# Kernel optimization log

Hardware: AMD Instinct MI355X
Metric: run time of the kernel (lower is better)

Reference implementation:

```python
import jax, jax.numpy as jnp
import numpy as np

B, L, D, DI, DS, DC, DTR = 128, 31, 1024, 2048, 16, 5, 64

def setup_inputs() -> dict:
    key = jax.random.key(0)
    ks = jax.random.split(key, 12)
    rn = lambda k, shp, s=0.02: jax.random.normal(k, shp, dtype=jnp.float32) * s
    return {
        "x": jax.random.normal(ks[0], (B, L, D), dtype=jnp.float32),
        "norm1_w": jnp.ones((D,), jnp.float32), "norm1_b": jnp.zeros((D,), jnp.float32),
        "in_proj_W": rn(ks[1], (2 * DI, D)),
        "conv_w": rn(ks[2], (DI, DC), 0.2), "conv_b": jnp.zeros((DI,), jnp.float32),
        "x_proj_W": rn(ks[3], (DTR + 2 * DS, DI)),
        "dt_proj_W": rn(ks[4], (DI, DTR), 0.1),
        "dt_proj_b": jnp.full((DI,), -4.6, dtype=jnp.float32),  # softplus^-1(~0.01)
        "A_log": jnp.tile(jnp.log(jnp.arange(1, DS + 1, dtype=jnp.float32))[None, :], (DI, 1)),
        "D_ssm": jnp.ones((DI,), jnp.float32),
        "out_proj_W": rn(ks[5], (D, DI)),
        "norm2_w": jnp.ones((D,), jnp.float32), "norm2_b": jnp.zeros((D,), jnp.float32),
        "ffn_W1": rn(ks[6], (2 * D, D)), "ffn_b1": jnp.zeros((2 * D,), jnp.float32),
        "ffn_W2": rn(ks[7], (D, 2 * D)), "ffn_b2": jnp.zeros((D,), jnp.float32),
        "cls_W1": rn(ks[8], (D, L * D)), "cls_b1": jnp.zeros((D,), jnp.float32),
        "cls_W2": rn(ks[9], (1, D)), "cls_b2": jnp.zeros((1,), jnp.float32),
    }

def _ln(x, w, b):
    m = x.mean(-1, keepdims=True)
    v = x.var(-1, keepdims=True)
    return (x - m) * jax.lax.rsqrt(v + 1e-5) * w + b

def _mamba(x, in_proj_W, conv_w, conv_b, x_proj_W, dt_proj_W, dt_proj_b, A_log, D_ssm, out_proj_W):
    # in_proj -> (u, z)
    xz = jnp.einsum('bld,ed->ble', x, in_proj_W)            # (B,L,2*DI)
    u, z = jnp.split(xz, 2, axis=-1)
    # causal depthwise conv1d (kernel DC) + SiLU
    xp = jnp.pad(u, ((0, 0), (DC - 1, 0), (0, 0)))
    uc = conv_b + sum(xp[:, k:k + L, :] * conv_w[:, k] for k in range(DC))
    uc = jax.nn.silu(uc)
    # input-dependent dt, B, C
    x_dbl = jnp.einsum('bld,ed->ble', uc, x_proj_W)         # (B,L,DTR+2*DS)
    dt, Bm, Cm = jnp.split(x_dbl, [DTR, DTR + DS], axis=-1)
    dt = jax.nn.softplus(jnp.einsum('blr,dr->bld', dt, dt_proj_W) + dt_proj_b)
    A = -jnp.exp(A_log)                                      # (DI,DS)
    def step(h, ins):
        dt_t, B_t, C_t, u_t = ins                            # (B,DI),(B,DS),(B,DS),(B,DI)
        dA = jnp.exp(dt_t[:, :, None] * A)                   # (B,DI,DS)
        h = h * dA + dt_t[:, :, None] * B_t[:, None, :] * u_t[:, :, None]
        y = jnp.einsum('bds,bs->bd', h, C_t)
        return h, y
    h0 = jnp.zeros((u.shape[0], DI, DS), u.dtype)
    _, ys = jax.lax.scan(step, h0, (dt.transpose(1, 0, 2), Bm.transpose(1, 0, 2),
                                    Cm.transpose(1, 0, 2), uc.transpose(1, 0, 2)))
    y = ys.transpose(1, 0, 2) + uc * D_ssm                   # skip term D*u
    y = y * jax.nn.silu(z)                                   # gate
    return jnp.einsum('bld,ed->ble', y, out_proj_W)

def reference(x, norm1_w, norm1_b, in_proj_W, conv_w, conv_b, x_proj_W, dt_proj_W,
              dt_proj_b, A_log, D_ssm, out_proj_W, norm2_w, norm2_b, ffn_W1, ffn_b1,
              ffn_W2, ffn_b2, cls_W1, cls_b1, cls_W2, cls_b2):
    # single encoder block (n_layers=1), dropout = identity (eval)
    res = x
    h = _ln(x, norm1_w, norm1_b)
    h = _mamba(h, in_proj_W, conv_w, conv_b, x_proj_W, dt_proj_W, dt_proj_b,
               A_log, D_ssm, out_proj_W)
    x = res + h
    res = x
    h = _ln(x, norm2_w, norm2_b)
    h = jax.nn.silu(jnp.einsum('bld,ed->ble', h, ffn_W1) + ffn_b1)
    h = jnp.einsum('ble,de->bld', h, ffn_W2) + ffn_b2
    x = res + h
    # classifier: Flatten -> Linear -> SiLU -> Linear
    flat = x.reshape(x.shape[0], -1)                          # (B, L*D)
    c = jax.nn.silu(flat @ cls_W1.T + cls_b1)
    out = c @ cls_W2.T + cls_b2                               # (B,1)
    return (out, x)
```

## Files before the change

### kernel.cpp

```cpp
#include <hip/hip_runtime.h>
#include <cstddef>
#include <cstdint>

#define B_   128
#define L_   31
#define D_   1024
#define DI_  2048
#define DS_  16
#define DC_  5
#define DTR_ 64
#define ROWS (B_ * L_)
#define KCLS (L_ * D_)

#define W_IN  0
#define W_OUT 4194304
#define W_F1  6291456
#define W_F2  8388608
#define W_XP  10485760
#define W_DT  10747904
#define WTOT  10878976

typedef unsigned short u16;
typedef __attribute__((ext_vector_type(8))) short s16x8;
typedef __attribute__((ext_vector_type(4))) float f32x4;

__device__ __forceinline__ float silu_f(float x) { return x / (1.0f + __expf(-x)); }

__device__ __forceinline__ u16 f2b(float f) {
    union { float f; uint32_t u; } c; c.f = f;
    uint32_t u = c.u + 0x7FFF + ((c.u >> 16) & 1);
    return (u16)(u >> 16);
}
__device__ __forceinline__ float b2f(u16 b) {
    union { uint32_t u; float f; } c; c.u = ((uint32_t)b) << 16;
    return c.f;
}
__device__ __forceinline__ uint32_t pack2(float lo, float hi) {
    return (uint32_t)f2b(lo) | ((uint32_t)f2b(hi) << 16);
}
__device__ __forceinline__ void cvt8(const float* __restrict__ s, u16* __restrict__ d) {
    const float4* p = (const float4*)s;
    float4 a = p[0], b = p[1];
    uint4 r;
    r.x = pack2(a.x, a.y); r.y = pack2(a.z, a.w);
    r.z = pack2(b.x, b.y); r.w = pack2(b.z, b.w);
    *(uint4*)d = r;
}

#define GLD16(g, s) __builtin_amdgcn_global_load_lds( \
    (const __attribute__((address_space(1))) void*)(g), \
    (__attribute__((address_space(3))) void*)(s), 16, 0, 0)

__global__ __launch_bounds__(256) void f2b_all_kernel(
    const float* __restrict__ inW, const float* __restrict__ outW,
    const float* __restrict__ f1W, const float* __restrict__ f2W,
    const float* __restrict__ xpW, const float* __restrict__ dtW,
    u16* __restrict__ wbuf)
{
    int g = blockIdx.x * 256 + threadIdx.x;
    if (g < 524288) { cvt8(inW + (size_t)g * 8, wbuf + W_IN + (size_t)g * 8); return; }
    g -= 524288;
    if (g < 262144) { cvt8(outW + (size_t)g * 8, wbuf + W_OUT + (size_t)g * 8); return; }
    g -= 262144;
    if (g < 262144) { cvt8(f1W + (size_t)g * 8, wbuf + W_F1 + (size_t)g * 8); return; }
    g -= 262144;
    if (g < 262144) { cvt8(f2W + (size_t)g * 8, wbuf + W_F2 + (size_t)g * 8); return; }
    g -= 262144;
    if (g < 32768) {
        const int row = g >> 8, col8 = (g & 255) * 8;
        u16* d = wbuf + W_XP + (size_t)row * 2048 + col8;
        if (row < 96) cvt8(xpW + (size_t)row * 2048 + col8, d);
        else *(uint4*)d = make_uint4(0, 0, 0, 0);
        return;
    }
    g -= 32768;
    if (g < 16384) cvt8(dtW + (size_t)g * 8, wbuf + W_DT + (size_t)g * 8);
}

__global__ __launch_bounds__(256) void ln_kernel(const float* __restrict__ x,
                                                 const float* __restrict__ w,
                                                 const float* __restrict__ b,
                                                 u16* __restrict__ y)
{
    const int row = blockIdx.x;
    const float* xr = x + (size_t)row * D_;
    float v[4];
    float sum = 0.f, sq = 0.f;
#pragma unroll
    for (int i = 0; i < 4; i++) {
        v[i] = xr[threadIdx.x + i * 256];
        sum += v[i];
        sq  += v[i] * v[i];
    }
#pragma unroll
    for (int o = 32; o > 0; o >>= 1) {
        sum += __shfl_down(sum, o, 64);
        sq  += __shfl_down(sq, o, 64);
    }
    __shared__ float red[8];
    const int wid = threadIdx.x >> 6;
    if ((threadIdx.x & 63) == 0) { red[wid] = sum; red[4 + wid] = sq; }
    __syncthreads();
    sum = red[0] + red[1] + red[2] + red[3];
    sq  = red[4] + red[5] + red[6] + red[7];
    const float mean = sum * (1.0f / D_);
    const float var  = sq * (1.0f / D_) - mean * mean;
    const float rstd = rsqrtf(var + 1e-5f);
    u16* yr = y + (size_t)row * D_;
#pragma unroll
    for (int i = 0; i < 4; i++) {
        const int c = threadIdx.x + i * 256;
        yr[c] = f2b((v[i] - mean) * rstd * w[c] + b[c]);
    }
}

__global__ __launch_bounds__(256) void ln2_fuse_kernel(const float* __restrict__ x,
                                                       const float* __restrict__ p0,
                                                       const float* __restrict__ p1,
                                                       const float* __restrict__ w,
                                                       const float* __restrict__ b,
                                                       float* __restrict__ x2,
                                                       u16* __restrict__ y)
{
    const int row = blockIdx.x;
    const size_t base = (size_t)row * D_;
    float v[4];
    float sum = 0.f, sq = 0.f;
#pragma unroll
    for (int i = 0; i < 4; i++) {
        const int c = threadIdx.x + i * 256;
        const float s = x[base + c] + p0[base + c] + p1[base + c];
        x2[base + c] = s;
        v[i] = s;
        sum += s;
        sq  += s * s;
    }
#pragma unroll
    for (int o = 32; o > 0; o >>= 1) {
        sum += __shfl_down(sum, o, 64);
        sq  += __shfl_down(sq, o, 64);
    }
    __shared__ float red[8];
    const int wid = threadIdx.x >> 6;
    if ((threadIdx.x & 63) == 0) { red[wid] = sum; red[4 + wid] = sq; }
    __syncthreads();
    sum = red[0] + red[1] + red[2] + red[3];
    sq  = red[4] + red[5] + red[6] + red[7];
    const float mean = sum * (1.0f / D_);
    const float var  = sq * (1.0f / D_) - mean * mean;
    const float rstd = rsqrtf(var + 1e-5f);
    u16* yr = y + base;
#pragma unroll
    for (int i = 0; i < 4; i++) {
        const int c = threadIdx.x + i * 256;
        yr[c] = f2b((v[i] - mean) * rstd * w[c] + b[c]);
    }
}

__global__ __launch_bounds__(256) void add3_bias_kernel(const float* __restrict__ x2,
                                                        const float* __restrict__ q0,
                                                        const float* __restrict__ q1,
                                                        const float* __restrict__ b2,
                                                        float* __restrict__ x3)
{
    const int i = blockIdx.x * 256 + threadIdx.x;
    float4 a  = ((const float4*)x2)[i];
    float4 c0 = ((const float4*)q0)[i];
    float4 c1 = ((const float4*)q1)[i];
    float4 bb = ((const float4*)b2)[i & 255];
    float4 r;
    r.x = a.x + c0.x + c1.x + bb.x;
    r.y = a.y + c0.y + c1.y + bb.y;
    r.z = a.z + c0.z + c1.z + bb.z;
    r.w = a.w + c0.w + c1.w + bb.w;
    ((float4*)x3)[i] = r;
}

template <int ACT, bool BIAS, bool RES, int OUT>
__global__ __launch_bounds__(256) void gemm_mfma(
    const u16* __restrict__ A, const u16* __restrict__ W,
    const float* __restrict__ bias, const float* __restrict__ res,
    void* __restrict__ Cout, int M, int K, int Nout, int kLen)
{
    __shared__ __align__(16) u16 As[128 * 32];
    __shared__ __align__(16) u16 Bs[128 * 32];
    const int tid = threadIdx.x;
    const int l = tid & 63, w = tid >> 6;
    const int bm = blockIdx.y * 128, bn = blockIdx.x * 128;
    const int kOff = blockIdx.z * kLen;

    const int sr = l >> 2;
    const int sk = (l & 3) * 8;
    const u16* gA = A + (size_t)(bm + w * 16 + sr) * K + kOff + sk;
    const u16* gB = W + (size_t)(bn + w * 16 + sr) * K + kOff + sk;
    u16* lA = As + (w * 16 + sr) * 32 + sk;
    u16* lB = Bs + (w * 16 + sr) * 32 + sk;

    const int lane15 = l & 15, lhi = l >> 4;
    const int wr = w >> 1, wc = w & 1;
    const u16* fA = As + (wr * 64 + lane15) * 32 + lhi * 8;
    const u16* fB = Bs + (wc * 64 + lane15) * 32 + lhi * 8;

    f32x4 acc[4][4] = {};

    for (int kk = 0; kk < kLen; kk += 32) {
        GLD16(gA, lA); GLD16(gA + (size_t)64 * K, lA + 64 * 32);
        GLD16(gB, lB); GLD16(gB + (size_t)64 * K, lB + 64 * 32);
        gA += 32; gB += 32;
        __syncthreads();
        s16x8 af[4], bfr[4];
#pragma unroll
        for (int mi = 0; mi < 4; mi++) af[mi]  = *(const s16x8*)(fA + mi * 16 * 32);
#pragma unroll
        for (int ni = 0; ni < 4; ni++) bfr[ni] = *(const s16x8*)(fB + ni * 16 * 32);
#pragma unroll
        for (int mi = 0; mi < 4; mi++)
#pragma unroll
            for (int ni = 0; ni < 4; ni++)
                acc[mi][ni] = __builtin_amdgcn_mfma_f32_16x16x32_bf16(
                    af[mi], bfr[ni], acc[mi][ni], 0, 0, 0);
        __syncthreads();
    }

#pragma unroll
    for (int ni = 0; ni < 4; ni++) {
        const int col = bn + wc * 64 + ni * 16 + lane15;
        if (col >= Nout) continue;
        const float bv = BIAS ? bias[col] : 0.0f;
#pragma unroll
        for (int mi = 0; mi < 4; mi++) {
#pragma unroll
            for (int r = 0; r < 4; r++) {
                const int row = bm + wr * 64 + mi * 16 + lhi * 4 + r;
                float v = acc[mi][ni][r] + bv;
                if (ACT == 1) v = silu_f(v);
                if (ACT == 2) v = (v > 20.0f) ? v : log1pf(__expf(v));
                if (RES) v += res[(size_t)row * Nout + col];
                if (OUT == 0) ((float*)Cout)[(size_t)row * Nout + col] = v;
                if (OUT == 1) ((u16*)Cout)[(size_t)row * Nout + col] = f2b(v);
                if (OUT == 2) atomicAdd(&((float*)Cout)[(size_t)row * Nout + col], v);
                if (OUT == 3) ((float*)Cout)[((size_t)blockIdx.z * M + row) * Nout + col] = v;
            }
        }
    }
}

#define KCH 512
__global__ __launch_bounds__(256) void gemm_cls_mfma(
    const float* __restrict__ A, const float* __restrict__ W,
    float* __restrict__ C)
{
    __shared__ __align__(16) u16 As[128 * 32];
    __shared__ __align__(16) u16 Bs[128 * 32];
    const int tid = threadIdx.x;
    const int l = tid & 63, w = tid >> 6;
    const int bn = blockIdx.x * 128;
    const int k0 = blockIdx.y * KCH;

    const int sr = l >> 2;
    const int sk = (l & 3) * 8;
    const int row = w * 16 + sr;
    const float* gA0 = A + (size_t)row * KCLS + k0 + sk;
    const float* gA1 = gA0 + (size_t)64 * KCLS;
    const float* gB0 = W + (size_t)(bn + row) * KCLS + k0 + sk;
    const float* gB1 = gB0 + (size_t)64 * KCLS;
    u16* lA0 = As + row * 32 + sk;  u16* lA1 = lA0 + 64 * 32;
    u16* lB0 = Bs + row * 32 + sk;  u16* lB1 = lB0 + 64 * 32;

    const int lane15 = l & 15, lhi = l >> 4;
    const int wr = w >> 1, wc = w & 1;
    const u16* fA = As + (wr * 64 + lane15) * 32 + lhi * 8;
    const u16* fB = Bs + (wc * 64 + lane15) * 32 + lhi * 8;

    f32x4 acc[4][4] = {};

    for (int ks = 0; ks < KCH / 32; ks++) {
        float4 a00 = *(const float4*)(gA0);     float4 a01 = *(const float4*)(gA0 + 4);
        float4 a10 = *(const float4*)(gA1);     float4 a11 = *(const float4*)(gA1 + 4);
        float4 b00 = *(const float4*)(gB0);     float4 b01 = *(const float4*)(gB0 + 4);
        float4 b10 = *(const float4*)(gB1);     float4 b11 = *(const float4*)(gB1 + 4);
        gA0 += 32; gA1 += 32; gB0 += 32; gB1 += 32;
        __syncthreads();
        uint4 r;
        r.x = pack2(a00.x, a00.y); r.y = pack2(a00.z, a00.w);
        r.z = pack2(a01.x, a01.y); r.w = pack2(a01.z, a01.w);
        *(uint4*)lA0 = r;
        r.x = pack2(a10.x, a10.y); r.y = pack2(a10.z, a10.w);
        r.z = pack2(a11.x, a11.y); r.w = pack2(a11.z, a11.w);
        *(uint4*)lA1 = r;
        r.x = pack2(b00.x, b00.y); r.y = pack2(b00.z, b00.w);
        r.z = pack2(b01.x, b01.y); r.w = pack2(b01.z, b01.w);
        *(uint4*)lB0 = r;
        r.x = pack2(b10.x, b10.y); r.y = pack2(b10.z, b10.w);
        r.z = pack2(b11.x, b11.y); r.w = pack2(b11.z, b11.w);
        *(uint4*)lB1 = r;
        __syncthreads();
        s16x8 af[4], bfr[4];
#pragma unroll
        for (int mi = 0; mi < 4; mi++) af[mi]  = *(const s16x8*)(fA + mi * 16 * 32);
#pragma unroll
        for (int ni = 0; ni < 4; ni++) bfr[ni] = *(const s16x8*)(fB + ni * 16 * 32);
#pragma unroll
        for (int mi = 0; mi < 4; mi++)
#pragma unroll
            for (int ni = 0; ni < 4; ni++)
                acc[mi][ni] = __builtin_amdgcn_mfma_f32_16x16x32_bf16(
                    af[mi], bfr[ni], acc[mi][ni], 0, 0, 0);
    }

#pragma unroll
    for (int ni = 0; ni < 4; ni++) {
        const int col = bn + wc * 64 + ni * 16 + lane15;
#pragma unroll
        for (int mi = 0; mi < 4; mi++) {
#pragma unroll
            for (int r = 0; r < 4; r++) {
                const int m = wr * 64 + mi * 16 + lhi * 4 + r;
                atomicAdd(&C[(size_t)m * 1024 + col], acc[mi][ni][r]);
            }
        }
    }
}

__global__ __launch_bounds__(256) void conv_silu_kernel(const u16* __restrict__ xz,
                                                        const float* __restrict__ cw,
                                                        const float* __restrict__ cb,
                                                        u16* __restrict__ uc)
{
    const int idx = blockIdx.x * 256 + threadIdx.x;
    const int d  = idx & (DI_ - 1);
    const int bl = idx >> 11;
    const int l  = bl % L_;
    const int b  = bl / L_;
    const u16* u = xz + (size_t)b * L_ * (2 * DI_) + d;
    float acc = cb[d];
#pragma unroll
    for (int k = 0; k < DC_; k++) {
        const int ll = l + k - (DC_ - 1);
        if (ll >= 0) acc = fmaf(b2f(u[(size_t)ll * (2 * DI_)]), cw[d * DC_ + k], acc);
    }
    uc[(size_t)bl * DI_ + d] = f2b(silu_f(acc));
}

__global__ __launch_bounds__(256) void dtext_kernel(const float* __restrict__ xdbl,
                                                    u16* __restrict__ dtb)
{
    const int idx = blockIdx.x * 256 + threadIdx.x;
    const int row = idx >> 4, c4 = (idx & 15) * 4;
    float4 v = *(const float4*)(xdbl + (size_t)row * 96 + c4);
    uint2 r;
    r.x = pack2(v.x, v.y); r.y = pack2(v.z, v.w);
    *(uint2*)(dtb + (size_t)row * 64 + c4) = r;
}

__global__ __launch_bounds__(256) void scan_kernel(const u16* __restrict__ dt,
                                                   const u16* __restrict__ uc,
                                                   const u16* __restrict__ xz,
                                                   const float* __restrict__ xdbl,
                                                   const float* __restrict__ A_log,
                                                   const float* __restrict__ D_ssm,
                                                   u16* __restrict__ y)
{
    const int idx = blockIdx.x * 256 + threadIdx.x;
    const int d = idx & (DI_ - 1);
    const int b = idx >> 11;
    float A[DS_];
#pragma unroll
    for (int s = 0; s < DS_; s++) A[s] = -__expf(A_log[d * DS_ + s]);
    const float Dv = D_ssm[d];
    float h[DS_] = {};
    for (int l = 0; l < L_; l++) {
        const size_t bl = (size_t)b * L_ + l;
        const float dtv = b2f(dt[bl * DI_ + d]);
        const float uv  = b2f(uc[bl * DI_ + d]);
        const float zv  = b2f(xz[bl * (2 * DI_) + DI_ + d]);
        const float* Bp = xdbl + bl * (DTR_ + 2 * DS_) + DTR_;
        const float* Cp = Bp + DS_;
        float yv = 0.f;
#pragma unroll
        for (int s = 0; s < DS_; s++) {
            h[s] = fmaf(h[s], __expf(dtv * A[s]), dtv * Bp[s] * uv);
            yv = fmaf(h[s], Cp[s], yv);
        }
        yv = fmaf(uv, Dv, yv);
        yv *= silu_f(zv);
        y[bl * DI_ + d] = f2b(yv);
    }
}

__global__ __launch_bounds__(256) void cls2_kernel(const float* __restrict__ c,
                                                   const float* __restrict__ b1,
                                                   const float* __restrict__ W2,
                                                   const float* __restrict__ b2,
                                                   float* __restrict__ out)
{
    const int b = blockIdx.x;
    float s = 0.f;
    for (int n = threadIdx.x; n < D_; n += 256) {
        float v = c[b * D_ + n] + b1[n];
        v = silu_f(v);
        s = fmaf(v, W2[n], s);
    }
#pragma unroll
    for (int o = 32; o > 0; o >>= 1) s += __shfl_down(s, o, 64);
    __shared__ float red[4];
    const int wid = threadIdx.x >> 6;
    if ((threadIdx.x & 63) == 0) red[wid] = s;
    __syncthreads();
    if (threadIdx.x == 0) out[b] = red[0] + red[1] + red[2] + red[3] + b2[0];
}

extern "C" void kernel_launch(void* const* d_in, const int* in_sizes, int n_in,
                              void* d_out, int out_size, void* d_ws, size_t ws_size,
                              hipStream_t stream)
{
    const float* x         = (const float*)d_in[0];
    const float* n1w       = (const float*)d_in[1];
    const float* n1b       = (const float*)d_in[2];
    const float* in_projW  = (const float*)d_in[3];
    const float* conv_w    = (const float*)d_in[4];
    const float* conv_b    = (const float*)d_in[5];
    const float* x_projW   = (const float*)d_in[6];
    const float* dt_projW  = (const float*)d_in[7];
    const float* dt_projb  = (const float*)d_in[8];
    const float* A_log     = (const float*)d_in[9];
    const float* D_ssm     = (const float*)d_in[10];
    const float* out_projW = (const float*)d_in[11];
    const float* n2w       = (const float*)d_in[12];
    const float* n2b       = (const float*)d_in[13];
    const float* ffn_W1    = (const float*)d_in[14];
    const float* ffn_b1    = (const float*)d_in[15];
    const float* ffn_W2    = (const float*)d_in[16];
    const float* ffn_b2    = (const float*)d_in[17];
    const float* cls_W1    = (const float*)d_in[18];
    const float* cls_b1    = (const float*)d_in[19];
    const float* cls_W2    = (const float*)d_in[20];
    const float* cls_b2    = (const float*)d_in[21];

    float* ws   = (float*)d_ws;
    u16*   xz_b = (u16*)ws;
    u16*   uc_b = xz_b + (size_t)ROWS * 4096;
    u16*   dt_b = uc_b + (size_t)ROWS * 2048;
    u16*   y_b  = dt_b + (size_t)ROWS * 2048;
    u16*   h_b  = y_b + (size_t)ROWS * 2048;
    float* x2   = (float*)(h_b + (size_t)ROWS * 1024);
    float* xdbl = x2 + (size_t)ROWS * 1024;
    u16*   dtb  = (u16*)(xdbl + (size_t)ROWS * 96);
    u16*   wbuf = dtb + (size_t)ROWS * 64;
    float* clsh = (float*)(wbuf + (size_t)WTOT);
    float* pq   = clsh + (size_t)B_ * D_;

    float* outv = (float*)d_out;
    float* x3   = outv + B_;

    f2b_all_kernel<<<dim3(5312), dim3(256), 0, stream>>>(
        in_projW, out_projW, ffn_W1, ffn_W2, x_projW, dt_projW, wbuf);
    ln_kernel<<<dim3(ROWS), dim3(256), 0, stream>>>(x, n1w, n1b, h_b);
    gemm_mfma<0, false, false, 1><<<dim3(32, 31, 1), dim3(256), 0, stream>>>(
        h_b, wbuf + W_IN, nullptr, nullptr, xz_b, ROWS, D_, 2 * DI_, D_);
    conv_silu_kernel<<<dim3(ROWS * DI_ / 256), dim3(256), 0, stream>>>(xz_b, conv_w, conv_b, uc_b);
    hipMemsetAsync(xdbl, 0, (size_t)ROWS * 96 * sizeof(float), stream);
    gemm_mfma<0, false, false, 2><<<dim3(1, 31, 16), dim3(256), 0, stream>>>(
        uc_b, wbuf + W_XP, nullptr, nullptr, xdbl, ROWS, DI_, DTR_ + 2 * DS_, 128);
    dtext_kernel<<<dim3(ROWS * 16 / 256), dim3(256), 0, stream>>>(xdbl, dtb);
    gemm_mfma<2, true, false, 1><<<dim3(16, 31, 1), dim3(256), 0, stream>>>(
        dtb, wbuf + W_DT, dt_projb, nullptr, dt_b, ROWS, DTR_, DI_, DTR_);
    scan_kernel<<<dim3(B_ * DI_ / 256), dim3(256), 0, stream>>>(
        dt_b, uc_b, xz_b, xdbl, A_log, D_ssm, y_b);
    gemm_mfma<0, false, false, 3><<<dim3(8, 31, 2), dim3(256), 0, stream>>>(
        y_b, wbuf + W_OUT, nullptr, nullptr, pq, ROWS, DI_, D_, 1024);
    ln2_fuse_kernel<<<dim3(ROWS), dim3(256), 0, stream>>>(
        x, pq, pq + (size_t)ROWS * D_, n2w, n2b, x2, h_b);
    gemm_mfma<1, true, false, 1><<<dim3(16, 31, 1), dim3(256), 0, stream>>>(
        h_b, wbuf + W_F1, ffn_b1, nullptr, uc_b, ROWS, D_, 2 * D_, D_);
    gemm_mfma<0, false, false, 3><<<dim3(8, 31, 2), dim3(256), 0, stream>>>(
        uc_b, wbuf + W_F2, nullptr, nullptr, pq, ROWS, 2 * D_, D_, 1024);
    add3_bias_kernel<<<dim3(ROWS * D_ / 4 / 256), dim3(256), 0, stream>>>(
        x2, pq, pq + (size_t)ROWS * D_, ffn_b2, x3);
    hipMemsetAsync(clsh, 0, (size_t)B_ * D_ * sizeof(float), stream);
    gemm_cls_mfma<<<dim3(1024 / 128, KCLS / KCH), dim3(256), 0, stream>>>(x3, cls_W1, clsh);
    cls2_kernel<<<dim3(B_), dim3(256), 0, stream>>>(clsh, cls_b1, cls_W2, cls_b2, outv);
}
```

Measured before the change: 425.6 us.

## Add double-buffered 256x256-tile MFMA GEMM for the large projections

Adds a new 512-thread GEMM kernel that computes 256x256 output tiles with 64-wide K steps. It double-buffers the LDS stages so global-to-LDS loads for the next K step overlap MFMA work on the current one. This kernel replaces the 128x128 GEMM for in_proj, out_proj, ffn1 and ffn2; the split-K GEMMs now use four partial slices, which the LN2 and bias-add kernels sum. Activation buffers are padded to 4096 rows so the tile loads stay in bounds. The cost is a 128KB LDS footprint that allows only one block per CU, fewer blocks for ffn1, possible LDS bank conflicts from the unpadded layout, and more partial-sum traffic.

```diff
diff --git a/kernel.cpp b/kernel.cpp
--- a/kernel.cpp
+++ b/kernel.cpp
@@ -10,6 +10,7 @@
 #define DC_  5
 #define DTR_ 64
 #define ROWS (B_ * L_)
+#define MPAD 4096
 #define KCLS (L_ * D_)
 
 #define W_IN  0
@@ -115,8 +116,7 @@
 }
 
 __global__ __launch_bounds__(256) void ln2_fuse_kernel(const float* __restrict__ x,
-                                                       const float* __restrict__ p0,
-                                                       const float* __restrict__ p1,
+                                                       const float* __restrict__ pq,
                                                        const float* __restrict__ w,
                                                        const float* __restrict__ b,
                                                        float* __restrict__ x2,
@@ -124,12 +124,17 @@
 {
     const int row = blockIdx.x;
     const size_t base = (size_t)row * D_;
+    const size_t PS = (size_t)ROWS * D_;
     float v[4];
     float sum = 0.f, sq = 0.f;
 #pragma unroll
     for (int i = 0; i < 4; i++) {
         const int c = threadIdx.x + i * 256;
-        const float s = x[base + c] + p0[base + c] + p1[base + c];
+        float s = x[base + c];
+        s += pq[base + c];
+        s += pq[PS + base + c];
+        s += pq[2 * PS + base + c];
+        s += pq[3 * PS + base + c];
         x2[base + c] = s;
         v[i] = s;
         sum += s;
@@ -157,30 +162,120 @@
     }
 }
 
-__global__ __launch_bounds__(256) void add3_bias_kernel(const float* __restrict__ x2,
-                                                        const float* __restrict__ q0,
-                                                        const float* __restrict__ q1,
+__global__ __launch_bounds__(256) void add4_bias_kernel(const float* __restrict__ x2,
+                                                        const float* __restrict__ pq,
                                                         const float* __restrict__ b2,
                                                         float* __restrict__ x3)
 {
     const int i = blockIdx.x * 256 + threadIdx.x;
+    const size_t PS4 = (size_t)ROWS * D_ / 4;
     float4 a  = ((const float4*)x2)[i];
-    float4 c0 = ((const float4*)q0)[i];
-    float4 c1 = ((const float4*)q1)[i];
+    float4 c0 = ((const float4*)pq)[i];
+    float4 c1 = ((const float4*)pq)[PS4 + i];
+    float4 c2 = ((const float4*)pq)[2 * PS4 + i];
+    float4 c3 = ((const float4*)pq)[3 * PS4 + i];
     float4 bb = ((const float4*)b2)[i & 255];
     float4 r;
-    r.x = a.x + c0.x + c1.x + bb.x;
-    r.y = a.y + c0.y + c1.y + bb.y;
-    r.z = a.z + c0.z + c1.z + bb.z;
-    r.w = a.w + c0.w + c1.w + bb.w;
+    r.x = a.x + c0.x + c1.x + c2.x + c3.x + bb.x;
+    r.y = a.y + c0.y + c1.y + c2.y + c3.y + bb.y;
+    r.z = a.z + c0.z + c1.z + c2.z + c3.z + bb.z;
+    r.w = a.w + c0.w + c1.w + c2.w + c3.w + bb.w;
     ((float4*)x3)[i] = r;
 }
 
-template <int ACT, bool BIAS, bool RES, int OUT>
+template <int ACT, bool BIAS, int OUT>
+__global__ __launch_bounds__(512, 2) void gemm256(
+    const u16* __restrict__ A, const u16* __restrict__ W,
+    const float* __restrict__ bias, void* __restrict__ Cout,
+    int K, int Nout, int kLen)
+{
+    __shared__ __align__(16) u16 As[2][256 * 64];
+    __shared__ __align__(16) u16 Bs[2][256 * 64];
+    const int tid = threadIdx.x;
+    const int l = tid & 63;
+    const int w = tid >> 6, wr = w >> 2, wc = w & 3;
+    const int lane15 = l & 15, lhi = l >> 4;
+    const int bm = blockIdx.y * 256, bn = blockIdx.x * 256;
+    const int kOff = blockIdx.z * kLen;
+
+    const int srow = tid >> 3;
+    const int skc  = (tid & 7) * 8;
+    const u16* gA = A + (size_t)(bm + srow) * K + kOff + skc;
+    const u16* gB = W + (size_t)(bn + srow) * K + kOff + skc;
+    const int soff = srow * 64 + skc;
+
+    const int NT = kLen / 64;
+    f32x4 acc[8][4] = {};
+
+#pragma unroll
+    for (int c = 0; c < 4; c++) {
+        GLD16(gA + (size_t)c * 64 * K, &As[0][c * 4096 + soff]);
+        GLD16(gB + (size_t)c * 64 * K, &Bs[0][c * 4096 + soff]);
+    }
+    __syncthreads();
+
+    for (int t = 0; t < NT; t++) {
+        const int cur = t & 1;
+        if (t + 1 < NT) {
+            const size_t go = (size_t)(t + 1) * 64;
+#pragma unroll
+            for (int c = 0; c < 4; c++) {
+                GLD16(gA + (size_t)c * 64 * K + go, &As[cur ^ 1][c * 4096 + soff]);
+                GLD16(gB + (size_t)c * 64 * K + go, &Bs[cur ^ 1][c * 4096 + soff]);
+            }
+        }
+        const u16* as = As[cur];
+        const u16* bs = Bs[cur];
+        s16x8 bf[2][4];
+#pragma unroll
+        for (int ks = 0; ks < 2; ks++)
+#pragma unroll
+            for (int ni = 0; ni < 4; ni++)
+                bf[ks][ni] = *(const s16x8*)(bs + (wc * 64 + ni * 16 + lane15) * 64 + ks * 32 + lhi * 8);
+#pragma unroll
+        for (int mh = 0; mh < 2; mh++) {
+            s16x8 af[2][4];
+#pragma unroll
+            for (int ks = 0; ks < 2; ks++)
+#pragma unroll
+                for (int mi = 0; mi < 4; mi++)
+                    af[ks][mi] = *(const s16x8*)(as + (wr * 128 + mh * 64 + mi * 16 + lane15) * 64 + ks * 32 + lhi * 8);
+#pragma unroll
+            for (int ks = 0; ks < 2; ks++)
+#pragma unroll
+                for (int mi = 0; mi < 4; mi++)
+#pragma unroll
+                    for (int ni = 0; ni < 4; ni++)
+                        acc[mh * 4 + mi][ni] = __builtin_amdgcn_mfma_f32_16x16x32_bf16(
+                            af[ks][mi], bf[ks][ni], acc[mh * 4 + mi][ni], 0, 0, 0);
+        }
+        __syncthreads();
+    }
+
+#pragma unroll
+    for (int ni = 0; ni < 4; ni++) {
+        const int col = bn + wc * 64 + ni * 16 + lane15;
+        const float bv = BIAS ? bias[col] : 0.0f;
+#pragma unroll
+        for (int mi8 = 0; mi8 < 8; mi8++) {
+#pragma unroll
+            for (int r = 0; r < 4; r++) {
+                const int row = bm + wr * 128 + mi8 * 16 + lhi * 4 + r;
+                if (row >= ROWS) continue;
+                float v = acc[mi8][ni][r] + bv;
+                if (ACT == 1) v = silu_f(v);
+                if (OUT == 1) ((u16*)Cout)[(size_t)row * Nout + col] = f2b(v);
+                else          ((float*)Cout)[((size_t)blockIdx.z * ROWS + row) * Nout + col] = v;
+            }
+        }
+    }
+}
+
+template <int ACT, bool BIAS, int OUT>
 __global__ __launch_bounds__(256) void gemm_mfma(
     const u16* __restrict__ A, const u16* __restrict__ W,
-    const float* __restrict__ bias, const float* __restrict__ res,
-    void* __restrict__ Cout, int M, int K, int Nout, int kLen)
+    const float* __restrict__ bias, void* __restrict__ Cout,
+    int M, int K, int Nout, int kLen)
 {
     __shared__ __align__(16) u16 As[128 * 32];
     __shared__ __align__(16) u16 Bs[128 * 32];
@@ -233,13 +328,9 @@
             for (int r = 0; r < 4; r++) {
                 const int row = bm + wr * 64 + mi * 16 + lhi * 4 + r;
                 float v = acc[mi][ni][r] + bv;
-                if (ACT == 1) v = silu_f(v);
                 if (ACT == 2) v = (v > 20.0f) ? v : log1pf(__expf(v));
-                if (RES) v += res[(size_t)row * Nout + col];
-                if (OUT == 0) ((float*)Cout)[(size_t)row * Nout + col] = v;
                 if (OUT == 1) ((u16*)Cout)[(size_t)row * Nout + col] = f2b(v);
                 if (OUT == 2) atomicAdd(&((float*)Cout)[(size_t)row * Nout + col], v);
-                if (OUT == 3) ((float*)Cout)[((size_t)blockIdx.z * M + row) * Nout + col] = v;
             }
         }
     }
@@ -437,16 +528,16 @@
     const float* cls_W2    = (const float*)d_in[20];
     const float* cls_b2    = (const float*)d_in[21];
 
-    float* ws   = (float*)d_ws;
-    u16*   xz_b = (u16*)ws;
-    u16*   uc_b = xz_b + (size_t)ROWS * 4096;
-    u16*   dt_b = uc_b + (size_t)ROWS * 2048;
-    u16*   y_b  = dt_b + (size_t)ROWS * 2048;
-    u16*   h_b  = y_b + (size_t)ROWS * 2048;
-    float* x2   = (float*)(h_b + (size_t)ROWS * 1024);
+    u16* base   = (u16*)d_ws;
+    u16* xz_b   = base;
+    u16* uc_b   = xz_b + (size_t)ROWS * 4096;
+    u16* dt_b   = uc_b + (size_t)MPAD * 2048;
+    u16* y_b    = dt_b + (size_t)ROWS * 2048;
+    u16* h_b    = y_b + (size_t)MPAD * 2048;
+    float* x2   = (float*)(h_b + (size_t)MPAD * 1024);
     float* xdbl = x2 + (size_t)ROWS * 1024;
-    u16*   dtb  = (u16*)(xdbl + (size_t)ROWS * 96);
-    u16*   wbuf = dtb + (size_t)ROWS * 64;
+    u16* dtb    = (u16*)(xdbl + (size_t)ROWS * 96);
+    u16* wbuf   = dtb + (size_t)ROWS * 64;
     float* clsh = (float*)(wbuf + (size_t)WTOT);
     float* pq   = clsh + (size_t)B_ * D_;
 
@@ -456,27 +547,26 @@
     f2b_all_kernel<<<dim3(5312), dim3(256), 0, stream>>>(
         in_projW, out_projW, ffn_W1, ffn_W2, x_projW, dt_projW, wbuf);
     ln_kernel<<<dim3(ROWS), dim3(256), 0, stream>>>(x, n1w, n1b, h_b);
-    gemm_mfma<0, false, false, 1><<<dim3(32, 31, 1), dim3(256), 0, stream>>>(
-        h_b, wbuf + W_IN, nullptr, nullptr, xz_b, ROWS, D_, 2 * DI_, D_);
+    gemm256<0, false, 1><<<dim3(16, 16, 1), dim3(512), 0, stream>>>(
+        h_b, wbuf + W_IN, nullptr, xz_b, D_, 2 * DI_, D_);
     conv_silu_kernel<<<dim3(ROWS * DI_ / 256), dim3(256), 0, stream>>>(xz_b, conv_w, conv_b, uc_b);
     hipMemsetAsync(xdbl, 0, (size_t)ROWS * 96 * sizeof(float), stream);
-    gemm_mfma<0, false, false, 2><<<dim3(1, 31, 16), dim3(256), 0, stream>>>(
-        uc_b, wbuf + W_XP, nullptr, nullptr, xdbl, ROWS, DI_, DTR_ + 2 * DS_, 128);
+    gemm_mfma<0, false, 2><<<dim3(1, 31, 16), dim3(256), 0, stream>>>(
+        uc_b, wbuf + W_XP, nullptr, xdbl, ROWS, DI_, DTR_ + 2 * DS_, 128);
     dtext_kernel<<<dim3(ROWS * 16 / 256), dim3(256), 0, stream>>>(xdbl, dtb);
-    gemm_mfma<2, true, false, 1><<<dim3(16, 31, 1), dim3(256), 0, stream>>>(
-        dtb, wbuf + W_DT, dt_projb, nullptr, dt_b, ROWS, DTR_, DI_, DTR_);
+    gemm_mfma<2, true, 1><<<dim3(16, 31, 1), dim3(256), 0, stream>>>(
+        dtb, wbuf + W_DT, dt_projb, dt_b, ROWS, DTR_, DI_, DTR_);
     scan_kernel<<<dim3(B_ * DI_ / 256), dim3(256), 0, stream>>>(
         dt_b, uc_b, xz_b, xdbl, A_log, D_ssm, y_b);
-    gemm_mfma<0, false, false, 3><<<dim3(8, 31, 2), dim3(256), 0, stream>>>(
-        y_b, wbuf + W_OUT, nullptr, nullptr, pq, ROWS, DI_, D_, 1024);
-    ln2_fuse_kernel<<<dim3(ROWS), dim3(256), 0, stream>>>(
-        x, pq, pq + (size_t)ROWS * D_, n2w, n2b, x2, h_b);
-    gemm_mfma<1, true, false, 1><<<dim3(16, 31, 1), dim3(256), 0, stream>>>(
-        h_b, wbuf + W_F1, ffn_b1, nullptr, uc_b, ROWS, D_, 2 * D_, D_);
-    gemm_mfma<0, false, false, 3><<<dim3(8, 31, 2), dim3(256), 0, stream>>>(
-        uc_b, wbuf + W_F2, nullptr, nullptr, pq, ROWS, 2 * D_, D_, 1024);
-    add3_bias_kernel<<<dim3(ROWS * D_ / 4 / 256), dim3(256), 0, stream>>>(
-        x2, pq, pq + (size_t)ROWS * D_, ffn_b2, x3);
+    gemm256<0, false, 3><<<dim3(4, 16, 4), dim3(512), 0, stream>>>(
+        y_b, wbuf + W_OUT, nullptr, pq, DI_, D_, 512);
+    ln2_fuse_kernel<<<dim3(ROWS), dim3(256), 0, stream>>>(x, pq, n2w, n2b, x2, h_b);
+    gemm256<1, true, 1><<<dim3(8, 16, 1), dim3(512), 0, stream>>>(
+        h_b, wbuf + W_F1, ffn_b1, uc_b, D_, 2 * D_, D_);
+    gemm256<0, false, 3><<<dim3(4, 16, 4), dim3(512), 0, stream>>>(
+        uc_b, wbuf + W_F2, nullptr, pq, 2 * D_, D_, 512);
+    add4_bias_kernel<<<dim3(ROWS * D_ / 4 / 256), dim3(256), 0, stream>>>(
+        x2, pq, ffn_b2, x3);
     hipMemsetAsync(clsh, 0, (size_t)B_ * D_ * sizeof(float), stream);
     gemm_cls_mfma<<<dim3(1024 / 128, KCLS / KCH), dim3(256), 0, stream>>>(x3, cls_W1, clsh);
     cls2_kernel<<<dim3(B_), dim3(256), 0, stream>>>(clsh, cls_b1, cls_W2, cls_b2, outv);
```

Measured after the change: 457.7 us. +7.5%, slower.

## Add BK=64 swizzled-LDS GEMM kernel for the large projection GEMMs

Applied to the files above, without the earlier changes.

Adds a new MFMA GEMM variant with a 64-wide K tile and XOR-swizzled shared-memory layout, and routes the in_proj, out_proj, and both FFN GEMMs through it. The larger K step halves the number of barrier pairs per output tile, and the swizzle is meant to avoid LDS bank conflicts on the fragment reads. The old gemm_mfma is kept for the small x_proj and dt_proj GEMMs, with its unused template paths removed. Shared memory per block doubles, which may lower occupancy.

```diff
diff --git a/kernel.cpp b/kernel.cpp
--- a/kernel.cpp
+++ b/kernel.cpp
@@ -176,11 +176,83 @@
     ((float4*)x3)[i] = r;
 }
 
-template <int ACT, bool BIAS, bool RES, int OUT>
+template <int ACT, bool BIAS, int OUT>
+__global__ __launch_bounds__(256) void gemm128_bk64(
+    const u16* __restrict__ A, const u16* __restrict__ W,
+    const float* __restrict__ bias, void* __restrict__ Cout,
+    int M, int K, int Nout, int kLen)
+{
+    __shared__ __align__(16) u16 As[128 * 64];
+    __shared__ __align__(16) u16 Bs[128 * 64];
+    const int tid = threadIdx.x;
+    const int l = tid & 63, w = tid >> 6;
+    const int bm = blockIdx.y * 128, bn = blockIdx.x * 128;
+    const int kOff = blockIdx.z * kLen;
+
+    const int srow = tid >> 3;
+    const int sg   = tid & 7;
+    const int sgx  = sg ^ (srow & 7);
+    const u16* gA = A + (size_t)(bm + srow) * K + kOff + sgx * 8;
+    const u16* gB = W + (size_t)(bn + srow) * K + kOff + sgx * 8;
+    const int soff = srow * 64 + sg * 8;
+
+    const int lane15 = l & 15, lhi = l >> 4;
+    const int key = lane15 & 7;
+    const int wr = w >> 1, wc = w & 1;
+    const u16* fArow = As + (wr * 64 + lane15) * 64;
+    const u16* fBrow = Bs + (wc * 64 + lane15) * 64;
+
+    f32x4 acc[4][4] = {};
+
+    for (int kk = 0; kk < kLen; kk += 64) {
+#pragma unroll
+        for (int c = 0; c < 4; c++) {
+            GLD16(gA + (size_t)c * 32 * K, As + c * 2048 + soff);
+            GLD16(gB + (size_t)c * 32 * K, Bs + c * 2048 + soff);
+        }
+        gA += 64; gB += 64;
+        __syncthreads();
+#pragma unroll
+        for (int ks = 0; ks < 2; ks++) {
+            const int gsel = ((ks * 4 + lhi) ^ key) * 8;
+            s16x8 af[4], bfr[4];
+#pragma unroll
+            for (int mi = 0; mi < 4; mi++) af[mi]  = *(const s16x8*)(fArow + mi * 16 * 64 + gsel);
+#pragma unroll
+            for (int ni = 0; ni < 4; ni++) bfr[ni] = *(const s16x8*)(fBrow + ni * 16 * 64 + gsel);
+#pragma unroll
+            for (int mi = 0; mi < 4; mi++)
+#pragma unroll
+                for (int ni = 0; ni < 4; ni++)
+                    acc[mi][ni] = __builtin_amdgcn_mfma_f32_16x16x32_bf16(
+                        af[mi], bfr[ni], acc[mi][ni], 0, 0, 0);
+        }
+        __syncthreads();
+    }
+
+#pragma unroll
+    for (int ni = 0; ni < 4; ni++) {
+        const int col = bn + wc * 64 + ni * 16 + lane15;
+        const float bv = BIAS ? bias[col] : 0.0f;
+#pragma unroll
+        for (int mi = 0; mi < 4; mi++) {
+#pragma unroll
+            for (int r = 0; r < 4; r++) {
+                const int row = bm + wr * 64 + mi * 16 + lhi * 4 + r;
+                float v = acc[mi][ni][r] + bv;
+                if (ACT == 1) v = silu_f(v);
+                if (OUT == 1) ((u16*)Cout)[(size_t)row * Nout + col] = f2b(v);
+                else          ((float*)Cout)[((size_t)blockIdx.z * M + row) * Nout + col] = v;
+            }
+        }
+    }
+}
+
+template <int ACT, bool BIAS, int OUT>
 __global__ __launch_bounds__(256) void gemm_mfma(
     const u16* __restrict__ A, const u16* __restrict__ W,
-    const float* __restrict__ bias, const float* __restrict__ res,
-    void* __restrict__ Cout, int M, int K, int Nout, int kLen)
+    const float* __restrict__ bias, void* __restrict__ Cout,
+    int M, int K, int Nout, int kLen)
 {
     __shared__ __align__(16) u16 As[128 * 32];
     __shared__ __align__(16) u16 Bs[128 * 32];
@@ -233,13 +305,9 @@
             for (int r = 0; r < 4; r++) {
                 const int row = bm + wr * 64 + mi * 16 + lhi * 4 + r;
                 float v = acc[mi][ni][r] + bv;
-                if (ACT == 1) v = silu_f(v);
                 if (ACT == 2) v = (v > 20.0f) ? v : log1pf(__expf(v));
-                if (RES) v += res[(size_t)row * Nout + col];
-                if (OUT == 0) ((float*)Cout)[(size_t)row * Nout + col] = v;
                 if (OUT == 1) ((u16*)Cout)[(size_t)row * Nout + col] = f2b(v);
                 if (OUT == 2) atomicAdd(&((float*)Cout)[(size_t)row * Nout + col], v);
-                if (OUT == 3) ((float*)Cout)[((size_t)blockIdx.z * M + row) * Nout + col] = v;
             }
         }
     }
@@ -437,16 +505,16 @@
     const float* cls_W2    = (const float*)d_in[20];
     const float* cls_b2    = (const float*)d_in[21];
 
-    float* ws   = (float*)d_ws;
-    u16*   xz_b = (u16*)ws;
-    u16*   uc_b = xz_b + (size_t)ROWS * 4096;
-    u16*   dt_b = uc_b + (size_t)ROWS * 2048;
-    u16*   y_b  = dt_b + (size_t)ROWS * 2048;
-    u16*   h_b  = y_b + (size_t)ROWS * 2048;
+    u16* base   = (u16*)d_ws;
+    u16* xz_b   = base;
+    u16* uc_b   = xz_b + (size_t)ROWS * 4096;
+    u16* dt_b   = uc_b + (size_t)ROWS * 2048;
+    u16* y_b    = dt_b + (size_t)ROWS * 2048;
+    u16* h_b    = y_b + (size_t)ROWS * 2048;
     float* x2   = (float*)(h_b + (size_t)ROWS * 1024);
     float* xdbl = x2 + (size_t)ROWS * 1024;
-    u16*   dtb  = (u16*)(xdbl + (size_t)ROWS * 96);
-    u16*   wbuf = dtb + (size_t)ROWS * 64;
+    u16* dtb    = (u16*)(xdbl + (size_t)ROWS * 96);
+    u16* wbuf   = dtb + (size_t)ROWS * 64;
     float* clsh = (float*)(wbuf + (size_t)WTOT);
     float* pq   = clsh + (size_t)B_ * D_;
 
@@ -456,25 +524,25 @@
     f2b_all_kernel<<<dim3(5312), dim3(256), 0, stream>>>(
         in_projW, out_projW, ffn_W1, ffn_W2, x_projW, dt_projW, wbuf);
     ln_kernel<<<dim3(ROWS), dim3(256), 0, stream>>>(x, n1w, n1b, h_b);
-    gemm_mfma<0, false, false, 1><<<dim3(32, 31, 1), dim3(256), 0, stream>>>(
-        h_b, wbuf + W_IN, nullptr, nullptr, xz_b, ROWS, D_, 2 * DI_, D_);
+    gemm128_bk64<0, false, 1><<<dim3(32, 31, 1), dim3(256), 0, stream>>>(
+        h_b, wbuf + W_IN, nullptr, xz_b, ROWS, D_, 2 * DI_, D_);
     conv_silu_kernel<<<dim3(ROWS * DI_ / 256), dim3(256), 0, stream>>>(xz_b, conv_w, conv_b, uc_b);
     hipMemsetAsync(xdbl, 0, (size_t)ROWS * 96 * sizeof(float), stream);
-    gemm_mfma<0, false, false, 2><<<dim3(1, 31, 16), dim3(256), 0, stream>>>(
-        uc_b, wbuf + W_XP, nullptr, nullptr, xdbl, ROWS, DI_, DTR_ + 2 * DS_, 128);
+    gemm_mfma<0, false, 2><<<dim3(1, 31, 16), dim3(256), 0, stream>>>(
+        uc_b, wbuf + W_XP, nullptr, xdbl, ROWS, DI_, DTR_ + 2 * DS_, 128);
     dtext_kernel<<<dim3(ROWS * 16 / 256), dim3(256), 0, stream>>>(xdbl, dtb);
-    gemm_mfma<2, true, false, 1><<<dim3(16, 31, 1), dim3(256), 0, stream>>>(
-        dtb, wbuf + W_DT, dt_projb, nullptr, dt_b, ROWS, DTR_, DI_, DTR_);
+    gemm_mfma<2, true, 1><<<dim3(16, 31, 1), dim3(256), 0, stream>>>(
+        dtb, wbuf + W_DT, dt_projb, dt_b, ROWS, DTR_, DI_, DTR_);
     scan_kernel<<<dim3(B_ * DI_ / 256), dim3(256), 0, stream>>>(
         dt_b, uc_b, xz_b, xdbl, A_log, D_ssm, y_b);
-    gemm_mfma<0, false, false, 3><<<dim3(8, 31, 2), dim3(256), 0, stream>>>(
-        y_b, wbuf + W_OUT, nullptr, nullptr, pq, ROWS, DI_, D_, 1024);
+    gemm128_bk64<0, false, 3><<<dim3(8, 31, 2), dim3(256), 0, stream>>>(
+        y_b, wbuf + W_OUT, nullptr, pq, ROWS, DI_, D_, 1024);
     ln2_fuse_kernel<<<dim3(ROWS), dim3(256), 0, stream>>>(
         x, pq, pq + (size_t)ROWS * D_, n2w, n2b, x2, h_b);
-    gemm_mfma<1, true, false, 1><<<dim3(16, 31, 1), dim3(256), 0, stream>>>(
-        h_b, wbuf + W_F1, ffn_b1, nullptr, uc_b, ROWS, D_, 2 * D_, D_);
-    gemm_mfma<0, false, false, 3><<<dim3(8, 31, 2), dim3(256), 0, stream>>>(
-        uc_b, wbuf + W_F2, nullptr, nullptr, pq, ROWS, 2 * D_, D_, 1024);
+    gemm128_bk64<1, true, 1><<<dim3(16, 31, 1), dim3(256), 0, stream>>>(
+        h_b, wbuf + W_F1, ffn_b1, uc_b, ROWS, D_, 2 * D_, D_);
+    gemm128_bk64<0, false, 3><<<dim3(8, 31, 2), dim3(256), 0, stream>>>(
+        uc_b, wbuf + W_F2, nullptr, pq, ROWS, 2 * D_, D_, 1024);
     add3_bias_kernel<<<dim3(ROWS * D_ / 4 / 256), dim3(256), 0, stream>>>(
         x2, pq, pq + (size_t)ROWS * D_, ffn_b2, x3);
     hipMemsetAsync(clsh, 0, (size_t)B_ * D_ * sizeof(float), stream);
```

After: 392.1 us. -7.9%, faster.
